# Kernel optimization log

Measured on AMD Instinct MI355X. Metric: run time of the kernel, lower is better.

The kernel has to match this reference:

```python
import jax, jax.numpy as jnp
import numpy as np

B, N, D = 16, 38400, 64      # batch, num_inputs (160*240), slot/feature size
S = 7                        # num_slots
MLP_H = 128                  # mlp_hidden_size (hard-coded in SlotAttentionModel)
ITERS = 3                    # num_iterations
EPS = 1e-8
LN_EPS = 1e-5


def _layernorm(x, g, b):
    m = jnp.mean(x, axis=-1, keepdims=True)
    v = jnp.var(x, axis=-1, keepdims=True)
    return (x - m) * jax.lax.rsqrt(v + LN_EPS) * g + b


def setup_inputs() -> dict:
    key = jax.random.key(0)
    ks = jax.random.split(key, 20)

    def lin(k, o, i):  # torch Linear weight [out, in], ~U-scale init
        return jax.random.normal(k, (o, i), jnp.float32) / np.sqrt(i)

    return {
        "inputs": jax.random.normal(ks[0], (B, N, D), jnp.float32),
        "slots_init": jax.random.normal(ks[1], (B, S, D), jnp.float32),
        "slots_mu": jax.random.normal(ks[2], (1, 1, D), jnp.float32) * 0.1,
        "slots_log_sigma": jax.random.normal(ks[3], (1, 1, D), jnp.float32) * 0.1,
        "ln_in_g": jnp.ones((D,), jnp.float32),
        "ln_in_b": jnp.zeros((D,), jnp.float32),
        "ln_slot_g": jnp.ones((D,), jnp.float32),
        "ln_slot_b": jnp.zeros((D,), jnp.float32),
        "ln_mlp_g": jnp.ones((D,), jnp.float32),
        "ln_mlp_b": jnp.zeros((D,), jnp.float32),
        "Wq": lin(ks[4], D, D),
        "Wk": lin(ks[5], D, D),
        "Wv": lin(ks[6], D, D),
        "W_ih": lin(ks[7], 3 * D, D),
        "W_hh": lin(ks[8], 3 * D, D),
        "b_ih": jnp.zeros((3 * D,), jnp.float32),
        "b_hh": jnp.zeros((3 * D,), jnp.float32),
        "W1": lin(ks[9], MLP_H, D),
        "b1": jnp.zeros((MLP_H,), jnp.float32),
        "W2": lin(ks[10], D, MLP_H),
        "b2": jnp.zeros((D,), jnp.float32),
    }


def reference(inputs, slots_init, slots_mu, slots_log_sigma,
              ln_in_g, ln_in_b, ln_slot_g, ln_slot_b, ln_mlp_g, ln_mlp_b,
              Wq, Wk, Wv, W_ih, W_hh, b_ih, b_hh, W1, b1, W2, b2):
    x = _layernorm(inputs, ln_in_g, ln_in_b)          # [B,N,D]
    k = x @ Wk.T                                      # [B,N,D]
    v = x @ Wv.T                                      # [B,N,D]

    slots = slots_mu + jnp.exp(slots_log_sigma) * slots_init  # [B,S,D]
    scale = D ** -0.5

    for _ in range(ITERS):
        slots_prev = slots
        s = _layernorm(slots, ln_slot_g, ln_slot_b)
        q = s @ Wq.T                                  # [B,S,D]
        # attn logits: [B,N,S], softmax over slots (competition for inputs)
        logits = scale * jnp.einsum('bnd,bsd->bns', k, q)
        attn = jax.nn.softmax(logits, axis=-1) + EPS
        attn = attn / jnp.sum(attn, axis=1, keepdims=True)  # weighted-mean norm over inputs
        updates = jnp.einsum('bns,bnd->bsd', attn, v)       # [B,S,D]

        # GRUCell(updates, slots_prev), torch gate order: r, z, n
        gi = updates @ W_ih.T + b_ih                  # [B,S,3D]
        gh = slots_prev @ W_hh.T + b_hh               # [B,S,3D]
        i_r, i_z, i_n = jnp.split(gi, 3, axis=-1)
        h_r, h_z, h_n = jnp.split(gh, 3, axis=-1)
        r = jax.nn.sigmoid(i_r + h_r)
        z = jax.nn.sigmoid(i_z + h_z)
        n = jnp.tanh(i_n + r * h_n)
        slots = (1.0 - z) * n + z * slots_prev

        # residual MLP refine
        m = _layernorm(slots, ln_mlp_g, ln_mlp_b)
        slots = slots + jax.nn.relu(m @ W1.T + b1) @ W2.T + b2

    return slots
```

## Files before the change

kernel.cpp:

```cpp
#include <hip/hip_runtime.h>

#define BB 16
#define NN 38400
#define DD 64
#define SS 7

__device__ __forceinline__ float wsum64(float v) {
#pragma unroll
  for (int off = 32; off > 0; off >>= 1) v += __shfl_xor(v, off);
  return v;
}

__global__ __launch_bounds__(64) void k_slot(
    int mode,
    const float* __restrict__ slots_init, const float* __restrict__ mu,
    const float* __restrict__ lsig,
    const float* __restrict__ ln_slot_g, const float* __restrict__ ln_slot_b,
    const float* __restrict__ ln_mlp_g, const float* __restrict__ ln_mlp_b,
    const float* __restrict__ ln_in_g, const float* __restrict__ ln_in_b,
    const float* __restrict__ Wq, const float* __restrict__ Wk,
    const float* __restrict__ Wv,
    const float* __restrict__ W_ih, const float* __restrict__ W_hh,
    const float* __restrict__ b_ih, const float* __restrict__ b_hh,
    const float* __restrict__ W1, const float* __restrict__ b1,
    const float* __restrict__ W2, const float* __restrict__ b2,
    float* __restrict__ slots, float* __restrict__ gqk,
    float* __restrict__ sc,
    float* __restrict__ ACC, float* __restrict__ ACCM, float* __restrict__ Zg,
    float* __restrict__ out)
{
  const int bs = blockIdx.x;
  const int b = bs / SS, s = bs % SS;
  const int d = threadIdx.x;
  __shared__ float t0[64], t1[64], hh[128];

  float slot;
  if (mode == 0) {
    slot = mu[d] + __expf(lsig[d]) * slots_init[bs * 64 + d];
  } else {
    const float zv = Zg[b * 8 + s];
    const float am = ACCM[b * 8 + s];
    const float ac = ACC[(b * 8 + s) * 64 + d];
    const float ubar = (ln_in_g[d] * (ac - am) + ln_in_b[d] * zv) / zv;
    t0[d] = ubar;
    __syncthreads();
    float upd = 0.f;
#pragma unroll
    for (int e = 0; e < 64; ++e) upd += t0[e] * Wv[d * 64 + e];
    const float sp = slots[bs * 64 + d];
    __syncthreads();
    t0[d] = upd;
    t1[d] = sp;
    __syncthreads();
    float s_r = b_ih[d] + b_hh[d];
    float s_z = b_ih[64 + d] + b_hh[64 + d];
    float i_n = b_ih[128 + d];
    float h_n = b_hh[128 + d];
#pragma unroll
    for (int e = 0; e < 64; ++e) {
      const float u = t0[e], p = t1[e];
      s_r += u * W_ih[d * 64 + e] + p * W_hh[d * 64 + e];
      s_z += u * W_ih[(64 + d) * 64 + e] + p * W_hh[(64 + d) * 64 + e];
      i_n += u * W_ih[(128 + d) * 64 + e];
      h_n += p * W_hh[(128 + d) * 64 + e];
    }
    const float rg = 1.f / (1.f + __expf(-s_r));
    const float zg = 1.f / (1.f + __expf(-s_z));
    const float ng = tanhf(i_n + rg * h_n);
    const float hv = (1.f - zg) * ng + zg * sp;
    const float mn = wsum64(hv) * (1.f / 64.f);
    const float dv = hv - mn;
    const float vr = wsum64(dv * dv) * (1.f / 64.f);
    const float rs = rsqrtf(vr + 1e-5f);
    const float mld = dv * rs * ln_mlp_g[d] + ln_mlp_b[d];
    __syncthreads();
    t0[d] = mld;
    __syncthreads();
    float h0 = b1[d], h1 = b1[64 + d];
#pragma unroll
    for (int e = 0; e < 64; ++e) {
      const float m = t0[e];
      h0 += m * W1[d * 64 + e];
      h1 += m * W1[(64 + d) * 64 + e];
    }
    hh[d] = fmaxf(h0, 0.f);
    hh[64 + d] = fmaxf(h1, 0.f);
    __syncthreads();
    float o = hv + b2[d];
#pragma unroll
    for (int j = 0; j < 128; ++j) o += hh[j] * W2[d * 128 + j];
    slot = o;
  }

  if (mode == 2) {
    out[bs * 64 + d] = slot;
    return;
  }
  slots[bs * 64 + d] = slot;

  const float mn = wsum64(slot) * (1.f / 64.f);
  const float dv = slot - mn;
  const float vr = wsum64(dv * dv) * (1.f / 64.f);
  const float rs = rsqrtf(vr + 1e-5f);
  const float sln = dv * rs * ln_slot_g[d] + ln_slot_b[d];
  __syncthreads();
  t0[d] = sln;
  __syncthreads();
  float q = 0.f;
#pragma unroll
  for (int e = 0; e < 64; ++e) q += t0[e] * Wq[d * 64 + e];
  __syncthreads();
  t1[d] = q;
  __syncthreads();
  float qe = 0.f;
#pragma unroll
  for (int dd = 0; dd < 64; ++dd) qe += t1[dd] * Wk[dd * 64 + d];
  qe *= 0.125f;
  const float gq = ln_in_g[d] * qe;
  gqk[(b * 8 + s) * 64 + d] = gq;
  const float sg = wsum64(gq);
  const float cb = wsum64(ln_in_b[d] * qe);
  if (d == 0) {
    sc[(b * 8 + s) * 2 + 0] = sg;
    sc[(b * 8 + s) * 2 + 1] = cb;
  }
  ACC[(b * 8 + s) * 64 + d] = 0.f;
  if (d == 0) {
    ACCM[b * 8 + s] = 0.f;
    Zg[b * 8 + s] = 0.f;
  }
}

__global__ __launch_bounds__(256) void k_main(
    const float* __restrict__ x,
    const float* __restrict__ gqk,
    const float* __restrict__ sc,
    float* __restrict__ ACC, float* __restrict__ ACCM, float* __restrict__ Zg)
{
  __shared__ __align__(16) float aa[8][256];
  __shared__ float wz[4][8], wm[4][8];
  const int t = threadIdx.x;
  const int b = blockIdx.y;
  const int row0 = blockIdx.x * 256;
  const float4* xr4 =
      reinterpret_cast<const float4*>(x + ((size_t)b * NN + row0 + t) * 64);

  const float* qb = gqk + b * 512;
  const float* scb = sc + b * 16;

  float lg[7];
#pragma unroll
  for (int s2 = 0; s2 < 7; ++s2) lg[s2] = 0.f;
  float sum = 0.f, sq = 0.f;
#pragma unroll
  for (int k = 0; k < 16; ++k) {
    const float4 v = xr4[k];
    sum += v.x + v.y + v.z + v.w;
    sq += v.x * v.x + v.y * v.y + v.z * v.z + v.w * v.w;
#pragma unroll
    for (int s2 = 0; s2 < 7; ++s2) {
      lg[s2] += v.x * qb[s2 * 64 + 4 * k + 0];
      lg[s2] += v.y * qb[s2 * 64 + 4 * k + 1];
      lg[s2] += v.z * qb[s2 * 64 + 4 * k + 2];
      lg[s2] += v.w * qb[s2 * 64 + 4 * k + 3];
    }
  }
  const float mean = sum * (1.f / 64.f);
  const float var = sq * (1.f / 64.f) - mean * mean;
  const float rstd = rsqrtf(var + 1e-5f);
  const float rm = rstd * mean;

  float mx = -1e30f;
#pragma unroll
  for (int s2 = 0; s2 < 7; ++s2) {
    lg[s2] = rstd * lg[s2] - rm * scb[s2 * 2] + scb[s2 * 2 + 1];
    mx = fmaxf(mx, lg[s2]);
  }
  float se = 0.f, ex[7];
#pragma unroll
  for (int s2 = 0; s2 < 7; ++s2) {
    ex[s2] = __expf(lg[s2] - mx);
    se += ex[s2];
  }
  const float inv = 1.f / se;
#pragma unroll
  for (int s2 = 0; s2 < 7; ++s2) {
    const float p = ex[s2] * inv + 1e-8f;
    aa[s2][t] = p * rstd;
    ex[s2] = p;
  }
  aa[7][t] = 0.f;

#pragma unroll
  for (int s2 = 0; s2 < 7; ++s2) {
    float z = ex[s2];
    float a = ex[s2] * rm;
#pragma unroll
    for (int off = 32; off > 0; off >>= 1) {
      z += __shfl_xor(z, off);
      a += __shfl_xor(a, off);
    }
    if ((t & 63) == 0) {
      wz[t >> 6][s2] = z;
      wm[t >> 6][s2] = a;
    }
  }
  __syncthreads();
  if (t < 7) {
    atomicAdd(&Zg[b * 8 + t], wz[0][t] + wz[1][t] + wz[2][t] + wz[3][t]);
    atomicAdd(&ACCM[b * 8 + t], wm[0][t] + wm[1][t] + wm[2][t] + wm[3][t]);
  }

  const int d = t & 63;
  const int s0 = t >> 6;
  const int s1 = s0 + 4;
  const float* xc = x + ((size_t)b * NN + row0) * 64 + d;
  float acc0 = 0.f, acc1 = 0.f;
#pragma unroll 4
  for (int n4 = 0; n4 < 64; ++n4) {
    const float4 p0 = *reinterpret_cast<const float4*>(&aa[s0][n4 * 4]);
    const float4 p1 = *reinterpret_cast<const float4*>(&aa[s1][n4 * 4]);
    const float x0 = xc[(n4 * 4 + 0) * 64];
    const float x1 = xc[(n4 * 4 + 1) * 64];
    const float x2 = xc[(n4 * 4 + 2) * 64];
    const float x3 = xc[(n4 * 4 + 3) * 64];
    acc0 += p0.x * x0;
    acc1 += p1.x * x0;
    acc0 += p0.y * x1;
    acc1 += p1.y * x1;
    acc0 += p0.z * x2;
    acc1 += p1.z * x2;
    acc0 += p0.w * x3;
    acc1 += p1.w * x3;
  }
  atomicAdd(&ACC[(b * 8 + s0) * 64 + d], acc0);
  atomicAdd(&ACC[(b * 8 + s1) * 64 + d], acc1);
}

extern "C" void kernel_launch(void* const* d_in, const int* in_sizes, int n_in,
                              void* d_out, int out_size, void* d_ws,
                              size_t ws_size, hipStream_t stream) {
  const float* inputs     = (const float*)d_in[0];
  const float* slots_init = (const float*)d_in[1];
  const float* slots_mu   = (const float*)d_in[2];
  const float* slots_lsig = (const float*)d_in[3];
  const float* ln_in_g    = (const float*)d_in[4];
  const float* ln_in_b    = (const float*)d_in[5];
  const float* ln_slot_g  = (const float*)d_in[6];
  const float* ln_slot_b  = (const float*)d_in[7];
  const float* ln_mlp_g   = (const float*)d_in[8];
  const float* ln_mlp_b   = (const float*)d_in[9];
  const float* Wq   = (const float*)d_in[10];
  const float* Wk   = (const float*)d_in[11];
  const float* Wv   = (const float*)d_in[12];
  const float* W_ih = (const float*)d_in[13];
  const float* W_hh = (const float*)d_in[14];
  const float* b_ih = (const float*)d_in[15];
  const float* b_hh = (const float*)d_in[16];
  const float* W1   = (const float*)d_in[17];
  const float* b1   = (const float*)d_in[18];
  const float* W2   = (const float*)d_in[19];
  const float* b2   = (const float*)d_in[20];

  float* ws    = (float*)d_ws;
  float* slots = ws;
  float* gqk   = ws + 7168;
  float* sc    = gqk + 8192;
  float* ACC   = sc + 256;
  float* ACCM  = ACC + 8192;
  float* Zg    = ACCM + 128;

  float* out = (float*)d_out;

#define SLOT_ARGS                                                          \
  slots_init, slots_mu, slots_lsig, ln_slot_g, ln_slot_b, ln_mlp_g,        \
      ln_mlp_b, ln_in_g, ln_in_b, Wq, Wk, Wv, W_ih, W_hh, b_ih, b_hh, W1,  \
      b1, W2, b2, slots, gqk, sc, ACC, ACCM, Zg, out

  k_slot<<<112, 64, 0, stream>>>(0, SLOT_ARGS);
  for (int it = 0; it < 3; ++it) {
    k_main<<<dim3(150, 16), 256, 0, stream>>>(inputs, gqk, sc, ACC, ACCM, Zg);
    k_slot<<<112, 64, 0, stream>>>(it == 2 ? 2 : 1, SLOT_ARGS);
  }
#undef SLOT_ARGS
}
```

Measured before the change: 238.0 us.

## Stage input tile in swizzled LDS and split rows across four threads

k_main now loads a 128-row tile of x into shared memory with coalesced float4 loads and an XOR swizzle, then reuses it for both the logit pass and the weighted accumulation instead of reading x from global memory twice. Each row's dot products are split across four lanes and combined with shuffles, and 512-thread blocks accumulate all 7 slots at once. This removes the second global pass over x and the strided per-row loads, at the cost of 32KB of LDS per block, which may limit occupancy, and twice as many blocks issuing atomics.

Result: slower. 369.9 us (+55.4%).

```diff
diff --git a/kernel.cpp b/kernel.cpp
--- a/kernel.cpp
+++ b/kernel.cpp
@@ -4,6 +4,7 @@
 #define NN 38400
 #define DD 64
 #define SS 7
+#define TILE 128
 
 __device__ __forceinline__ float wsum64(float v) {
 #pragma unroll
@@ -106,11 +107,11 @@
   __syncthreads();
   t0[d] = sln;
   __syncthreads();
-  float q = 0.f;
-#pragma unroll
-  for (int e = 0; e < 64; ++e) q += t0[e] * Wq[d * 64 + e];
-  __syncthreads();
-  t1[d] = q;
+  float qv = 0.f;
+#pragma unroll
+  for (int e = 0; e < 64; ++e) qv += t0[e] * Wq[d * 64 + e];
+  __syncthreads();
+  t1[d] = qv;
   __syncthreads();
   float qe = 0.f;
 #pragma unroll
@@ -131,39 +132,54 @@
   }
 }
 
-__global__ __launch_bounds__(256) void k_main(
+__global__ __launch_bounds__(512, 8) void k_main(
     const float* __restrict__ x,
     const float* __restrict__ gqk,
     const float* __restrict__ sc,
     float* __restrict__ ACC, float* __restrict__ ACCM, float* __restrict__ Zg)
 {
-  __shared__ __align__(16) float aa[8][256];
-  __shared__ float wz[4][8], wm[4][8];
+  __shared__ __align__(16) float xs[TILE * 64];
+  __shared__ __align__(16) float pa[7 * TILE];
+  __shared__ float wz[8][8], wm[8][8];
   const int t = threadIdx.x;
   const int b = blockIdx.y;
-  const int row0 = blockIdx.x * 256;
-  const float4* xr4 =
-      reinterpret_cast<const float4*>(x + ((size_t)b * NN + row0 + t) * 64);
-
+  const int row0 = blockIdx.x * TILE;
+
+  const float4* src =
+      reinterpret_cast<const float4*>(x + ((size_t)b * NN + row0) * 64);
+#pragma unroll
+  for (int i = 0; i < 4; ++i) {
+    const int f = i * 512 + t;
+    const float4 v = src[f];
+    const int r = f >> 4, c = f & 15;
+    *reinterpret_cast<float4*>(&xs[(r << 6) + ((c ^ (r & 15)) << 2)]) = v;
+  }
   const float* qb = gqk + b * 512;
   const float* scb = sc + b * 16;
-
-  float lg[7];
-#pragma unroll
-  for (int s2 = 0; s2 < 7; ++s2) lg[s2] = 0.f;
+  __syncthreads();
+
+  const int row = t >> 2, q = t & 3;
+  float lg[7] = {0.f, 0.f, 0.f, 0.f, 0.f, 0.f, 0.f};
   float sum = 0.f, sq = 0.f;
 #pragma unroll
-  for (int k = 0; k < 16; ++k) {
-    const float4 v = xr4[k];
+  for (int j = 0; j < 4; ++j) {
+    const int c = q * 4 + j;
+    const float4 v = *reinterpret_cast<const float4*>(
+        &xs[(row << 6) + ((c ^ (row & 15)) << 2)]);
     sum += v.x + v.y + v.z + v.w;
     sq += v.x * v.x + v.y * v.y + v.z * v.z + v.w * v.w;
 #pragma unroll
     for (int s2 = 0; s2 < 7; ++s2) {
-      lg[s2] += v.x * qb[s2 * 64 + 4 * k + 0];
-      lg[s2] += v.y * qb[s2 * 64 + 4 * k + 1];
-      lg[s2] += v.z * qb[s2 * 64 + 4 * k + 2];
-      lg[s2] += v.w * qb[s2 * 64 + 4 * k + 3];
-    }
+      const float4 g4 = *reinterpret_cast<const float4*>(&qb[s2 * 64 + c * 4]);
+      lg[s2] += v.x * g4.x + v.y * g4.y + v.z * g4.z + v.w * g4.w;
+    }
+  }
+#pragma unroll
+  for (int off = 1; off <= 2; off <<= 1) {
+    sum += __shfl_xor(sum, off);
+    sq += __shfl_xor(sq, off);
+#pragma unroll
+    for (int s2 = 0; s2 < 7; ++s2) lg[s2] += __shfl_xor(lg[s2], off);
   }
   const float mean = sum * (1.f / 64.f);
   const float var = sq * (1.f / 64.f) - mean * mean;
@@ -176,27 +192,26 @@
     lg[s2] = rstd * lg[s2] - rm * scb[s2 * 2] + scb[s2 * 2 + 1];
     mx = fmaxf(mx, lg[s2]);
   }
-  float se = 0.f, ex[7];
+  float se = 0.f;
 #pragma unroll
   for (int s2 = 0; s2 < 7; ++s2) {
-    ex[s2] = __expf(lg[s2] - mx);
-    se += ex[s2];
+    lg[s2] = __expf(lg[s2] - mx);
+    se += lg[s2];
   }
   const float inv = 1.f / se;
 #pragma unroll
+  for (int s2 = 0; s2 < 7; ++s2) lg[s2] = lg[s2] * inv + 1e-8f;
+
+  if (q == 0) {
+#pragma unroll
+    for (int s2 = 0; s2 < 7; ++s2) pa[s2 * TILE + row] = lg[s2] * rstd;
+  }
+#pragma unroll
   for (int s2 = 0; s2 < 7; ++s2) {
-    const float p = ex[s2] * inv + 1e-8f;
-    aa[s2][t] = p * rstd;
-    ex[s2] = p;
-  }
-  aa[7][t] = 0.f;
-
-#pragma unroll
-  for (int s2 = 0; s2 < 7; ++s2) {
-    float z = ex[s2];
-    float a = ex[s2] * rm;
-#pragma unroll
-    for (int off = 32; off > 0; off >>= 1) {
+    float z = lg[s2];
+    float a = lg[s2] * rm;
+#pragma unroll
+    for (int off = 4; off <= 32; off <<= 1) {
       z += __shfl_xor(z, off);
       a += __shfl_xor(a, off);
     }
@@ -207,34 +222,33 @@
   }
   __syncthreads();
   if (t < 7) {
-    atomicAdd(&Zg[b * 8 + t], wz[0][t] + wz[1][t] + wz[2][t] + wz[3][t]);
-    atomicAdd(&ACCM[b * 8 + t], wm[0][t] + wm[1][t] + wm[2][t] + wm[3][t]);
-  }
-
-  const int d = t & 63;
-  const int s0 = t >> 6;
-  const int s1 = s0 + 4;
-  const float* xc = x + ((size_t)b * NN + row0) * 64 + d;
-  float acc0 = 0.f, acc1 = 0.f;
+    float z = 0.f, a = 0.f;
+#pragma unroll
+    for (int w = 0; w < 8; ++w) {
+      z += wz[w][t];
+      a += wm[w][t];
+    }
+    atomicAdd(&Zg[b * 8 + t], z);
+    atomicAdd(&ACCM[b * 8 + t], a);
+  }
+
+  const int s = t >> 6;
+  if (s < 7) {
+    const int d = t & 63;
+    const int ch = d >> 2, sub = d & 3;
+    const float* pas = pa + s * TILE;
+    float acc = 0.f;
 #pragma unroll 4
-  for (int n4 = 0; n4 < 64; ++n4) {
-    const float4 p0 = *reinterpret_cast<const float4*>(&aa[s0][n4 * 4]);
-    const float4 p1 = *reinterpret_cast<const float4*>(&aa[s1][n4 * 4]);
-    const float x0 = xc[(n4 * 4 + 0) * 64];
-    const float x1 = xc[(n4 * 4 + 1) * 64];
-    const float x2 = xc[(n4 * 4 + 2) * 64];
-    const float x3 = xc[(n4 * 4 + 3) * 64];
-    acc0 += p0.x * x0;
-    acc1 += p1.x * x0;
-    acc0 += p0.y * x1;
-    acc1 += p1.y * x1;
-    acc0 += p0.z * x2;
-    acc1 += p1.z * x2;
-    acc0 += p0.w * x3;
-    acc1 += p1.w * x3;
-  }
-  atomicAdd(&ACC[(b * 8 + s0) * 64 + d], acc0);
-  atomicAdd(&ACC[(b * 8 + s1) * 64 + d], acc1);
+    for (int n4 = 0; n4 < TILE / 4; ++n4) {
+      const float4 p4 = *reinterpret_cast<const float4*>(&pas[n4 * 4]);
+      const int n = n4 * 4;
+      acc += p4.x * xs[((n + 0) << 6) + ((ch ^ ((n + 0) & 15)) << 2) + sub];
+      acc += p4.y * xs[((n + 1) << 6) + ((ch ^ ((n + 1) & 15)) << 2) + sub];
+      acc += p4.z * xs[((n + 2) << 6) + ((ch ^ ((n + 2) & 15)) << 2) + sub];
+      acc += p4.w * xs[((n + 3) << 6) + ((ch ^ ((n + 3) & 15)) << 2) + sub];
+    }
+    atomicAdd(&ACC[(b * 8 + s) * 64 + d], acc);
+  }
 }
 
 extern "C" void kernel_launch(void* const* d_in, const int* in_sizes, int n_in,
@@ -279,7 +293,8 @@
 
   k_slot<<<112, 64, 0, stream>>>(0, SLOT_ARGS);
   for (int it = 0; it < 3; ++it) {
-    k_main<<<dim3(150, 16), 256, 0, stream>>>(inputs, gqk, sc, ACC, ACCM, Zg);
+    k_main<<<dim3(NN / TILE, BB), 512, 0, stream>>>(inputs, gqk, sc, ACC,
+                                                    ACCM, Zg);
     k_slot<<<112, 64, 0, stream>>>(it == 2 ? 2 : 1, SLOT_ARGS);
   }
 #undef SLOT_ARGS
```
